# Kernel optimization log

Measured on AMD Instinct MI355X. Metric: run time of the kernel, lower is better.

The kernel has to match this reference:

```python
import jax, jax.numpy as jnp
import numpy as np

H = 1024
B, S = 8, 2048
EPS = 1e-5


def _layernorm(x, w, b):
    m = jnp.mean(x, axis=-1, keepdims=True)
    v = jnp.mean((x - m) ** 2, axis=-1, keepdims=True)
    return (x - m) * jax.lax.rsqrt(v + EPS) * w + b


def setup_inputs() -> dict:
    key = jax.random.key(0)
    ks = jax.random.split(key, 10)
    x = jax.random.normal(ks[0], (B, S, H), dtype=jnp.float32)
    # LayerNorm params (torch default init: weight=1, bias=0)
    qn_w = jnp.ones((H,), jnp.float32)
    qn_b = jnp.zeros((H,), jnp.float32)
    kvn_w = jnp.ones((H,), jnp.float32)
    kvn_b = jnp.zeros((H,), jnp.float32)
    # q_prime/k_prime/v_prime ~ U(-0.5, 0.5)
    q_prime = jax.random.uniform(ks[1], (1, H), jnp.float32) - 0.5
    k_prime = jax.random.uniform(ks[2], (1, H), jnp.float32) - 0.5
    v_prime = jax.random.uniform(ks[3], (1, H), jnp.float32) - 0.5
    # Linear params, torch-style fan_in init
    lim = 1.0 / np.sqrt(H)
    qW = jax.random.uniform(ks[4], (H, H), jnp.float32, -lim, lim)
    qb = jax.random.uniform(ks[5], (H,), jnp.float32, -lim, lim)
    v1W = jax.random.uniform(ks[6], (H, H), jnp.float32, -lim, lim)
    v1b = jax.random.uniform(ks[7], (H,), jnp.float32, -lim, lim)
    v2W = jax.random.uniform(ks[8], (H, H), jnp.float32, -lim, lim)
    v2b = jax.random.uniform(ks[9], (H,), jnp.float32, -lim, lim)
    return {"x": x, "qn_w": qn_w, "qn_b": qn_b, "kvn_w": kvn_w, "kvn_b": kvn_b,
            "q_prime": q_prime, "k_prime": k_prime, "v_prime": v_prime,
            "qW": qW, "qb": qb, "v1W": v1W, "v1b": v1b, "v2W": v2W, "v2b": v2b}


def reference(x, qn_w, qn_b, kvn_w, kvn_b, q_prime, k_prime, v_prime,
              qW, qb, v1W, v1b, v2W, v2b):
    divisor = jnp.sqrt(jnp.float32(x.shape[-1]))
    xqn = _layernorm(x, qn_w, qn_b)            # [B,S,H]
    xkvn = _layernorm(x, kvn_w, kvn_b)         # [B,S,H]
    kr = xkvn * jax.nn.sigmoid(k_prime)        # [B,S,H]
    qr = (xqn @ qW.T + qb) * jax.nn.sigmoid(q_prime)  # [B,S,H]
    vp = jax.nn.sigmoid(v_prime)               # [1,H]
    gate = jax.nn.sigmoid(vp @ v1W.T + v1b) * jnp.tanh(vp @ v2W.T + v2b)  # [1,H]
    vr = xkvn * gate                           # [B,S,H]
    scores = jnp.einsum('bsh,bth->bst', qr, kr) / divisor  # [B,S,S]
    b, s, t = scores.shape
    # global softmax over flattened seq x seq matrix
    attn = jax.nn.softmax(scores.reshape(b, s * t), axis=-1).reshape(b, s, t)
    attended = jnp.einsum('bst,bth->bsh', attn, vr)
    return attended + xqn
```

## Files before the change

kernel.cpp:

```cpp
#include <hip/hip_runtime.h>
#include <stdint.h>


#define DEVI __device__ __forceinline__

typedef __bf16 bf16x8 __attribute__((ext_vector_type(8)));
typedef float  f32x4  __attribute__((ext_vector_type(4)));

typedef __attribute__((address_space(3))) uint32_t lds_u32_t;
typedef __attribute__((address_space(1))) uint32_t glb_u32_t;

DEVI uint16_t f2bf(float f) {
  union { float f; uint32_t u; } v; v.f = f;
  uint32_t r = (v.u + 0x7fffu + ((v.u >> 16) & 1u)) >> 16;
  return (uint16_t)r;
}
DEVI float bf2f(uint16_t b) {
  union { uint32_t u; float f; } v; v.u = ((uint32_t)b) << 16;
  return v.f;
}
DEVI float sigm(float x) { return 1.0f / (1.0f + __expf(-x)); }

DEVI void gl_lds16(const void* g, const void* lds_base) {
  __builtin_amdgcn_global_load_lds((glb_u32_t*)(uintptr_t)g,
                                   (lds_u32_t*)(uint32_t)(uintptr_t)lds_base,
                                   16, 0, 0);
}


#define SLOT (256 * 32)

DEVI void stage_half(const uint16_t* __restrict__ src, size_t ld, int kbase,
                     uint16_t* slot, int tid) {
#pragma unroll
  for (int q = 0; q < 2; q++) {
    const int idx = q * 512 + tid;
    const int r = idx >> 2;
    const int cl = (((idx & 3) ^ ((r >> 1) & 3)) * 8);
    gl_lds16(src + (size_t)r * ld + (kbase + cl),
             slot + (size_t)(q * 512 + (tid & ~63)) * 8);
  }
}

DEVI void gemm256(const uint16_t* __restrict__ A, size_t lda,
                  const uint16_t* __restrict__ B, size_t ldb,
                  int K, uint16_t* sA, uint16_t* sB, f32x4 (&acc)[8][4])
{
  const int tid = threadIdx.x, lane = tid & 63, w = tid >> 6;
  const int wr = (w >> 2) * 128, wc = (w & 3) * 64;
  const int m16 = lane & 15, quad = lane >> 4;
  const int NT = K >> 6, NH = K >> 5;

  stage_half(B, ldb, 0, sB, tid);
  stage_half(A, lda, 0, sA, tid);
  stage_half(B, ldb, 32, sB + SLOT, tid);
  stage_half(A, lda, 32, sA + SLOT, tid);
  stage_half(B, ldb, 64, sB + 2 * SLOT, tid);
  stage_half(A, lda, 64, sA + 2 * SLOT, tid);
  asm volatile("s_waitcnt vmcnt(4)" ::: "memory");
  __builtin_amdgcn_s_barrier();

  const int sw = (quad ^ ((m16 >> 1) & 3)) * 8;

  for (int t = 0; t < NT; t++) {
#pragma unroll
    for (int ks = 0; ks < 2; ks++) {
      const uint16_t* a_s = sA + ((2 * t + ks) & 3) * SLOT;
      const uint16_t* b_s = sB + ((2 * t + ks) & 3) * SLOT;
      const int h = 2 * t + 3 + ks;

      bf16x8 bv[4], af[4];
#pragma unroll
      for (int i = 0; i < 4; i++)
        bv[i] = *(const bf16x8*)(b_s + (wc + i * 16 + m16) * 32 + sw);
#pragma unroll
      for (int i = 0; i < 4; i++)
        af[i] = *(const bf16x8*)(a_s + (wr + i * 16 + m16) * 32 + sw);
      if (h < NH) stage_half(B, ldb, h * 32, sB + (h & 3) * SLOT, tid);
      __builtin_amdgcn_s_barrier();
      __builtin_amdgcn_s_setprio(1);
#pragma unroll
      for (int mi = 0; mi < 4; mi++)
#pragma unroll
        for (int ni = 0; ni < 4; ni++)
          acc[mi][ni] = __builtin_amdgcn_mfma_f32_16x16x32_bf16(
              af[mi], bv[ni], acc[mi][ni], 0, 0, 0);
      __builtin_amdgcn_s_setprio(0);

      bf16x8 af2[4];
#pragma unroll
      for (int i = 0; i < 4; i++)
        af2[i] = *(const bf16x8*)(a_s + (wr + 64 + i * 16 + m16) * 32 + sw);
      if (h < NH) stage_half(A, lda, h * 32, sA + (h & 3) * SLOT, tid);
      if (ks == 1) {
        if (t < NT - 2) asm volatile("s_waitcnt vmcnt(4)" ::: "memory");
        else            asm volatile("s_waitcnt vmcnt(0)" ::: "memory");
      }
      __builtin_amdgcn_s_barrier();
      __builtin_amdgcn_s_setprio(1);
#pragma unroll
      for (int mi = 0; mi < 4; mi++)
#pragma unroll
        for (int ni = 0; ni < 4; ni++)
          acc[4 + mi][ni] = __builtin_amdgcn_mfma_f32_16x16x32_bf16(
              af2[mi], bv[ni], acc[4 + mi][ni], 0, 0, 0);
      __builtin_amdgcn_s_setprio(0);
    }
  }
}

__global__ void gatecvt_kernel(const float* __restrict__ qW, uint16_t* __restrict__ qWbf,
                               const float* __restrict__ v_prime,
                               const float* __restrict__ v1W, const float* __restrict__ v1b,
                               const float* __restrict__ v2W, const float* __restrict__ v2b,
                               const float* __restrict__ k_prime,
                               float* __restrict__ gate2)
{
  const int bid = blockIdx.x;
  if (bid < 1024) {
    size_t i = ((size_t)bid * 256 + threadIdx.x) * 4;
    float4 v = *(const float4*)(qW + i);
    *(ushort4*)(qWbf + i) = make_ushort4(f2bf(v.x), f2bf(v.y), f2bf(v.z), f2bf(v.w));
    return;
  }
  const int tid = threadIdx.x, lane = tid & 63, w = tid >> 6;
  const int j = (bid - 1024) * 4 + w;
  float d1 = 0.f, d2 = 0.f;
  for (int it = 0; it < 16; it++) {
    int i = it * 64 + lane;
    float vp = sigm(v_prime[i]);
    d1 += vp * v1W[(size_t)j * 1024 + i];
    d2 += vp * v2W[(size_t)j * 1024 + i];
  }
  for (int off = 32; off; off >>= 1) { d1 += __shfl_xor(d1, off); d2 += __shfl_xor(d2, off); }
  if (lane == 0)
    gate2[j] = sigm(d1 + v1b[j]) * tanhf(d2 + v2b[j]) / sigm(k_prime[j]);
}

__global__ __launch_bounds__(256) void ln_kernel(
    const float* __restrict__ x,
    const float* __restrict__ qn_w, const float* __restrict__ qn_b,
    const float* __restrict__ kvn_w, const float* __restrict__ kvn_b,
    const float* __restrict__ k_prime,
    uint16_t* __restrict__ xqn_bf, uint16_t* __restrict__ kr,
    float* __restrict__ krowsq, float* __restrict__ qnormsq)
{
  if (blockIdx.x < 64) qnormsq[blockIdx.x * 256 + threadIdx.x] = 0.f;

  const int lane = threadIdx.x & 63, w = threadIdx.x >> 6;
  const int row = blockIdx.x * 4 + w;
  const float4* xr = (const float4*)(x + (size_t)row * 1024);
  float4 v[4];
  float s = 0.f, sq = 0.f;
#pragma unroll
  for (int i = 0; i < 4; i++) {
    v[i] = xr[i * 64 + lane];
    s  += v[i].x + v[i].y + v[i].z + v[i].w;
    sq += v[i].x * v[i].x + v[i].y * v[i].y + v[i].z * v[i].z + v[i].w * v[i].w;
  }
  for (int off = 32; off; off >>= 1) { s += __shfl_xor(s, off); sq += __shfl_xor(sq, off); }
  const float mean = s * (1.f / 1024.f);
  const float rstd = rsqrtf(sq * (1.f / 1024.f) - mean * mean + 1e-5f);

  float ksq = 0.f;
  const size_t o4 = (size_t)row * 256;
#pragma unroll
  for (int i = 0; i < 4; i++) {
    const int idx = i * 64 + lane;
    float4 qw = ((const float4*)qn_w)[idx],  qb4 = ((const float4*)qn_b)[idx];
    float4 kw = ((const float4*)kvn_w)[idx], kb4 = ((const float4*)kvn_b)[idx];
    float4 kp = ((const float4*)k_prime)[idx];
    float xn0 = (v[i].x - mean) * rstd, xn1 = (v[i].y - mean) * rstd;
    float xn2 = (v[i].z - mean) * rstd, xn3 = (v[i].w - mean) * rstd;
    float xq0 = xn0 * qw.x + qb4.x, xq1 = xn1 * qw.y + qb4.y;
    float xq2 = xn2 * qw.z + qb4.z, xq3 = xn3 * qw.w + qb4.w;
    float xk0 = xn0 * kw.x + kb4.x, xk1 = xn1 * kw.y + kb4.y;
    float xk2 = xn2 * kw.z + kb4.z, xk3 = xn3 * kw.w + kb4.w;
    float k0 = xk0 * sigm(kp.x), k1 = xk1 * sigm(kp.y);
    float k2 = xk2 * sigm(kp.z), k3 = xk3 * sigm(kp.w);
    ksq += k0 * k0 + k1 * k1 + k2 * k2 + k3 * k3;
    ((ushort4*)xqn_bf)[o4 + idx] = make_ushort4(f2bf(xq0), f2bf(xq1), f2bf(xq2), f2bf(xq3));
    ((ushort4*)kr)[o4 + idx] = make_ushort4(f2bf(k0), f2bf(k1), f2bf(k2), f2bf(k3));
  }
  for (int off = 32; off; off >>= 1) ksq += __shfl_xor(ksq, off);
  if (lane == 0) krowsq[row] = ksq;
}

__global__ __launch_bounds__(512, 2) void qr_gemm_kernel(
    const uint16_t* __restrict__ xqn_bf, const uint16_t* __restrict__ qWbf,
    const float* __restrict__ qb, const float* __restrict__ q_prime,
    uint16_t* __restrict__ qr, float* __restrict__ qnormsq)
{
  __shared__ uint16_t sA[4 * SLOT], sB[4 * SLOT];
  const int lid = blockIdx.x;
  const int c = lid >> 6, r = lid & 63;
  f32x4 acc[8][4];
#pragma unroll
  for (int i = 0; i < 8; i++)
#pragma unroll
    for (int j = 0; j < 4; j++) acc[i][j] = (f32x4)0.0f;

  gemm256(xqn_bf + (size_t)r * 256 * 1024, 1024,
          qWbf + (size_t)c * 256 * 1024, 1024, 1024, sA, sB, acc);

  const int tid = threadIdx.x, lane = tid & 63, w = tid >> 6;
  const int m16 = lane & 15, quad = lane >> 4;
  const int rbase = r * 256 + (w >> 2) * 128, cbase = c * 256 + (w & 3) * 64;
#pragma unroll
  for (int ai = 0; ai < 8; ai++) {
    const int gr0 = rbase + (ai >> 2) * 64 + (ai & 3) * 16 + quad * 4;
    float rsq[4] = {0.f, 0.f, 0.f, 0.f};
#pragma unroll
    for (int ni = 0; ni < 4; ni++) {
      const int gc = cbase + ni * 16 + m16;
      const float scale = sigm(q_prime[gc]);
      const float bias = qb[gc];
#pragma unroll
      for (int rr = 0; rr < 4; rr++) {
        float val = (acc[ai][ni][rr] + bias) * scale;
        qr[(size_t)(gr0 + rr) * 1024 + gc] = f2bf(val);
        rsq[rr] += val * val;
      }
    }
#pragma unroll
    for (int rr = 0; rr < 4; rr++) {
      float tq = rsq[rr];
      tq += __shfl_xor(tq, 1); tq += __shfl_xor(tq, 2);
      tq += __shfl_xor(tq, 4); tq += __shfl_xor(tq, 8);
      if (m16 == 0) atomicAdd(&qnormsq[gr0 + rr], tq);
    }
  }
}

__global__ void transpose_kernel(const uint16_t* __restrict__ kr,
                                 const float* __restrict__ gate2,
                                 uint16_t* __restrict__ vrt)
{
  __shared__ uint16_t t[64 * 72];
  const int b = blockIdx.z;
  const int t0 = blockIdx.x * 64, h0 = blockIdx.y * 64;
  const uint16_t* src = kr + (size_t)b * 2048 * 1024;
#pragma unroll
  for (int p = 0; p < 2; p++) {
    int flat = p * 256 + threadIdx.x;
    int r = flat >> 3, c = (flat & 7) * 8;
    *(uint4*)(&t[r * 72 + c]) = *(const uint4*)(src + (size_t)(t0 + r) * 1024 + h0 + c);
  }
  __syncthreads();
  uint16_t* dst = vrt + (size_t)b * 1024 * 2048;
#pragma unroll
  for (int p = 0; p < 2; p++) {
    int flat = p * 256 + threadIdx.x;
    int oh = flat >> 3, oc = (flat & 7) * 8;
    const float g = gate2[h0 + oh];
    union { uint16_t e[8]; uint4 v; } u;
#pragma unroll
    for (int j = 0; j < 8; j++) u.e[j] = f2bf(bf2f(t[(oc + j) * 72 + oh]) * g);
    *(uint4*)(dst + (size_t)(h0 + oh) * 2048 + t0 + oc) = u.v;
  }
}

__global__ __launch_bounds__(512, 2) void scores_kernel(
    const uint16_t* __restrict__ qr, const uint16_t* __restrict__ kr,
    const float* __restrict__ qnormsq, const float* __restrict__ krowsq,
    uint16_t* __restrict__ scores, float* __restrict__ blockZ)
{
  __shared__ uint16_t sA[4 * SLOT], sB[4 * SLOT];
  __shared__ float redz[8], rm[8], rk[8], sMhat;
  const int lid = blockIdx.x;
  const int b = lid >> 6, c = (lid >> 3) & 7, r = lid & 7;
  const int tid = threadIdx.x, lane = tid & 63, w = tid >> 6;

  {
    float mq = 0.f, mk = 0.f;
    for (int i = tid; i < 2048; i += 512) {
      mq = fmaxf(mq, qnormsq[b * 2048 + i]);
      mk = fmaxf(mk, krowsq[b * 2048 + i]);
    }
    for (int off = 32; off; off >>= 1) {
      mq = fmaxf(mq, __shfl_xor(mq, off));
      mk = fmaxf(mk, __shfl_xor(mk, off));
    }
    if (lane == 0) { rm[w] = mq; rk[w] = mk; }
    __syncthreads();
    if (tid == 0) {
      float qmax = rm[0], kmax = rk[0];
#pragma unroll
      for (int i = 1; i < 8; i++) { qmax = fmaxf(qmax, rm[i]); kmax = fmaxf(kmax, rk[i]); }
      sMhat = sqrtf(qmax * kmax) * 0.03125f;
    }
  }

  f32x4 acc[8][4];
#pragma unroll
  for (int i = 0; i < 8; i++)
#pragma unroll
    for (int j = 0; j < 4; j++) acc[i][j] = (f32x4)0.0f;

  gemm256(qr + (size_t)b * 2048 * 1024 + (size_t)r * 256 * 1024, 1024,
          kr + (size_t)b * 2048 * 1024 + (size_t)c * 256 * 1024, 1024,
          1024, sA, sB, acc);

  const float Mhat = sMhat;
  const int m16 = lane & 15, quad = lane >> 4;
  const int rbase = r * 256 + (w >> 2) * 128, cbase = c * 256 + (w & 3) * 64;
  uint16_t* S = scores + ((size_t)b << 22);
  float zt = 0.f;
#pragma unroll
  for (int ai = 0; ai < 8; ai++) {
    const int gr0 = rbase + (ai >> 2) * 64 + (ai & 3) * 16 + quad * 4;
#pragma unroll
    for (int ni = 0; ni < 4; ni++) {
      const int gc = cbase + ni * 16 + m16;
#pragma unroll
      for (int rr = 0; rr < 4; rr++) {
        float pe = __expf(acc[ai][ni][rr] * 0.03125f - Mhat);
        zt += pe;
        S[(size_t)(gr0 + rr) * 2048 + gc] = f2bf(pe);
      }
    }
  }
  for (int off = 32; off; off >>= 1) zt += __shfl_xor(zt, off);
  if (lane == 0) redz[w] = zt;
  __syncthreads();
  if (tid == 0) {
    float sz = 0.f;
#pragma unroll
    for (int i = 0; i < 8; i++) sz += redz[i];
    blockZ[lid] = sz;
  }
}

__global__ __launch_bounds__(512, 2) void pv_gemm_kernel(
    const uint16_t* __restrict__ P, const uint16_t* __restrict__ vrt,
    const float* __restrict__ blockZ, const uint16_t* __restrict__ xqn_bf,
    float* __restrict__ out)
{
  __shared__ uint16_t sA[4 * SLOT], sB[4 * SLOT];
  __shared__ float sZ;
  const int lid = blockIdx.x;
  const int b = lid >> 5, c = (lid >> 3) & 3, r = lid & 7;
  const int tid = threadIdx.x;

  if (tid < 64) {
    float z = blockZ[b * 64 + tid];
    for (int off = 32; off; off >>= 1) z += __shfl_xor(z, off);
    if (tid == 0) sZ = z;
  }

  f32x4 acc[8][4];
#pragma unroll
  for (int i = 0; i < 8; i++)
#pragma unroll
    for (int j = 0; j < 4; j++) acc[i][j] = (f32x4)0.0f;

  gemm256(P + ((size_t)b << 22) + (size_t)r * 256 * 2048, 2048,
          vrt + (size_t)b * 1024 * 2048 + (size_t)c * 256 * 2048, 2048,
          2048, sA, sB, acc);

  const float invZ = 1.0f / sZ;
  const int lane = tid & 63, w = tid >> 6;
  const int m16 = lane & 15, quad = lane >> 4;
  const int rbase = r * 256 + (w >> 2) * 128, cbase = c * 256 + (w & 3) * 64;
#pragma unroll
  for (int ai = 0; ai < 8; ai++) {
    const int gr0 = rbase + (ai >> 2) * 64 + (ai & 3) * 16 + quad * 4;
#pragma unroll
    for (int ni = 0; ni < 4; ni++) {
      const int gc = cbase + ni * 16 + m16;
#pragma unroll
      for (int rr = 0; rr < 4; rr++) {
        size_t o = ((size_t)b * 2048 + gr0 + rr) * 1024 + gc;
        out[o] = acc[ai][ni][rr] * invZ + bf2f(xqn_bf[o]);
      }
    }
  }
}

extern "C" void kernel_launch(void* const* d_in, const int* in_sizes, int n_in,
                              void* d_out, int out_size, void* d_ws, size_t ws_size,
                              hipStream_t stream) {
  const float* x       = (const float*)d_in[0];
  const float* qn_w    = (const float*)d_in[1];
  const float* qn_b    = (const float*)d_in[2];
  const float* kvn_w   = (const float*)d_in[3];
  const float* kvn_b   = (const float*)d_in[4];
  const float* q_prime = (const float*)d_in[5];
  const float* k_prime = (const float*)d_in[6];
  const float* v_prime = (const float*)d_in[7];
  const float* qW      = (const float*)d_in[8];
  const float* qb      = (const float*)d_in[9];
  const float* v1W     = (const float*)d_in[10];
  const float* v1b     = (const float*)d_in[11];
  const float* v2W     = (const float*)d_in[12];
  const float* v2b     = (const float*)d_in[13];
  float* out = (float*)d_out;

  const size_t BS = 16384, H = 1024;
  char* ws = (char*)d_ws;
  size_t off = 0;
  auto alloc = [&](size_t bytes) -> char* {
    char* p = ws + off;
    off = (off + bytes + 255) & ~(size_t)255;
    return p;
  };
  float*    gate2   = (float*)alloc(H * 4);
  float*    blockZ  = (float*)alloc(2048 * 4);
  float*    qnormsq = (float*)alloc(16384 * 4);
  float*    krowsq  = (float*)alloc(16384 * 4);
  uint16_t* qWbf    = (uint16_t*)alloc(H * H * 2);
  uint16_t* xqn_bf  = (uint16_t*)alloc(BS * H * 2);
  uint16_t* kr      = (uint16_t*)alloc(BS * H * 2);
  uint16_t* scores  = (uint16_t*)alloc(BS * H * 2 * 2);
  uint16_t* vrt     = (uint16_t*)alloc(BS * H * 2);
  uint16_t* qr      = (uint16_t*)alloc(BS * H * 2);

  gatecvt_kernel<<<1280, 256, 0, stream>>>(qW, qWbf, v_prime, v1W, v1b, v2W, v2b,
                                           k_prime, gate2);
  ln_kernel<<<4096, 256, 0, stream>>>(x, qn_w, qn_b, kvn_w, kvn_b, k_prime,
                                      xqn_bf, kr, krowsq, qnormsq);
  qr_gemm_kernel<<<256, 512, 0, stream>>>(xqn_bf, qWbf, qb, q_prime, qr, qnormsq);
  transpose_kernel<<<dim3(32, 16, 8), 256, 0, stream>>>(kr, gate2, vrt);
  scores_kernel<<<512, 512, 0, stream>>>(qr, kr, qnormsq, krowsq, scores, blockZ);
  pv_gemm_kernel<<<256, 512, 0, stream>>>(scores, vrt, blockZ, xqn_bf, out);
}
```

Baseline: 358.4 us.

## Use double-buffered GEMM in scores kernel to raise occupancy

Replaces the 4-slot, deeper-pipelined GEMM in the scores kernel with a simpler double-buffered loop that prefetches the next K-slice while computing the current one. LDS usage is halved and launch bounds are raised to request 4 blocks per CU, aiming for more occupancy to hide latency. In exchange, prefetch depth drops to one slice with a full vmcnt(0) wait and barrier every iteration. Register pressure under 512 threads x 4 blocks may force spills given the 128 accumulator registers per thread.

```diff
diff --git a/kernel.cpp b/kernel.cpp
--- a/kernel.cpp
+++ b/kernel.cpp
@@ -26,7 +26,6 @@
                                    (lds_u32_t*)(uint32_t)(uintptr_t)lds_base,
                                    16, 0, 0);
 }
-
 
 #define SLOT (256 * 32)
 
@@ -105,6 +104,64 @@
           acc[4 + mi][ni] = __builtin_amdgcn_mfma_f32_16x16x32_bf16(
               af2[mi], bv[ni], acc[4 + mi][ni], 0, 0, 0);
       __builtin_amdgcn_s_setprio(0);
+    }
+  }
+}
+
+DEVI void gemm256_r2(const uint16_t* __restrict__ A, size_t lda,
+                     const uint16_t* __restrict__ B, size_t ldb,
+                     int K, uint16_t* sA, uint16_t* sB, f32x4 (&acc)[8][4])
+{
+  const int tid = threadIdx.x, lane = tid & 63, w = tid >> 6;
+  const int wr = (w >> 2) * 128, wc = (w & 3) * 64;
+  const int m16 = lane & 15, quad = lane >> 4;
+  const int NH = K >> 5;
+
+  stage_half(B, ldb, 0, sB, tid);
+  stage_half(A, lda, 0, sA, tid);
+  asm volatile("s_waitcnt vmcnt(0)" ::: "memory");
+  __builtin_amdgcn_s_barrier();
+
+  const int sw = (quad ^ ((m16 >> 1) & 3)) * 8;
+
+  for (int h = 0; h < NH; h++) {
+    const uint16_t* a_s = sA + (h & 1) * SLOT;
+    const uint16_t* b_s = sB + (h & 1) * SLOT;
+
+    if (h + 1 < NH) {
+      stage_half(B, ldb, (h + 1) * 32, sB + ((h + 1) & 1) * SLOT, tid);
+      stage_half(A, lda, (h + 1) * 32, sA + ((h + 1) & 1) * SLOT, tid);
+    }
+
+    bf16x8 bv[4], af[4], af2[4];
+#pragma unroll
+    for (int i = 0; i < 4; i++)
+      bv[i] = *(const bf16x8*)(b_s + (wc + i * 16 + m16) * 32 + sw);
+#pragma unroll
+    for (int i = 0; i < 4; i++)
+      af[i] = *(const bf16x8*)(a_s + (wr + i * 16 + m16) * 32 + sw);
+#pragma unroll
+    for (int i = 0; i < 4; i++)
+      af2[i] = *(const bf16x8*)(a_s + (wr + 64 + i * 16 + m16) * 32 + sw);
+
+    __builtin_amdgcn_s_setprio(1);
+#pragma unroll
+    for (int mi = 0; mi < 4; mi++)
+#pragma unroll
+      for (int ni = 0; ni < 4; ni++)
+        acc[mi][ni] = __builtin_amdgcn_mfma_f32_16x16x32_bf16(
+            af[mi], bv[ni], acc[mi][ni], 0, 0, 0);
+#pragma unroll
+    for (int mi = 0; mi < 4; mi++)
+#pragma unroll
+      for (int ni = 0; ni < 4; ni++)
+        acc[4 + mi][ni] = __builtin_amdgcn_mfma_f32_16x16x32_bf16(
+            af2[mi], bv[ni], acc[4 + mi][ni], 0, 0, 0);
+    __builtin_amdgcn_s_setprio(0);
+
+    if (h + 1 < NH) {
+      asm volatile("s_waitcnt vmcnt(0)" ::: "memory");
+      __builtin_amdgcn_s_barrier();
     }
   }
 }
@@ -260,12 +317,12 @@
   }
 }
 
-__global__ __launch_bounds__(512, 2) void scores_kernel(
+__global__ __launch_bounds__(512, 4) void scores_kernel(
     const uint16_t* __restrict__ qr, const uint16_t* __restrict__ kr,
     const float* __restrict__ qnormsq, const float* __restrict__ krowsq,
     uint16_t* __restrict__ scores, float* __restrict__ blockZ)
 {
-  __shared__ uint16_t sA[4 * SLOT], sB[4 * SLOT];
+  __shared__ uint16_t sA[2 * SLOT], sB[2 * SLOT];
   __shared__ float redz[8], rm[8], rk[8], sMhat;
   const int lid = blockIdx.x;
   const int b = lid >> 6, c = (lid >> 3) & 7, r = lid & 7;
@@ -297,9 +354,9 @@
 #pragma unroll
     for (int j = 0; j < 4; j++) acc[i][j] = (f32x4)0.0f;
 
-  gemm256(qr + (size_t)b * 2048 * 1024 + (size_t)r * 256 * 1024, 1024,
-          kr + (size_t)b * 2048 * 1024 + (size_t)c * 256 * 1024, 1024,
-          1024, sA, sB, acc);
+  gemm256_r2(qr + (size_t)b * 2048 * 1024 + (size_t)r * 256 * 1024, 1024,
+             kr + (size_t)b * 2048 * 1024 + (size_t)c * 256 * 1024, 1024,
+             1024, sA, sB, acc);
 
   const float Mhat = sMhat;
   const int m16 = lane & 15, quad = lane >> 4;
```

Result: slower. 938.1 us (+161.7%).
